# Kernel optimization log

Measured on AMD Instinct MI355X. Metric: run time of the kernel, lower is better.

Reference implementation:

```python
import jax, jax.numpy as jnp
import numpy as np

B, T, IN, OUT = 32, 2048, 1024, 256
DT = 1.0
TAU_MIN, TAU_MAX = 15.0, 25.0


def setup_inputs() -> dict:
    key = jax.random.key(0)
    k1, k2, k3 = jax.random.split(key, 3)
    inputs = jax.random.normal(k1, (B, T, IN), dtype=jnp.float32)
    bound = float(np.sqrt(1.0 / IN))
    weight = jax.random.uniform(k2, (OUT, IN), minval=-bound, maxval=bound, dtype=jnp.float32)
    bias = jnp.zeros((OUT,), dtype=jnp.float32)
    tau = jax.random.uniform(k3, (OUT,), minval=TAU_MIN, maxval=TAU_MAX, dtype=jnp.float32)
    decay = jnp.exp(-DT / tau)  # per-channel leak alpha in (0,1)
    return {"inputs": inputs, "weight": weight, "bias": bias, "decay": decay}


def reference(inputs, weight, bias, decay):
    # Dense projection: [B,T,IN] @ [IN,OUT] -> [B,T,OUT]
    current = jnp.einsum("bti,oi->bto", inputs, weight) + bias
    # Leaky integrator: u_t = alpha * u_{t-1} + (1-alpha) * x_t, u_0 = 0
    one_minus = 1.0 - decay

    def step(u, x):  # u,x: [B,OUT]
        u = decay * u + one_minus * x
        return u, u

    u0 = jnp.zeros((inputs.shape[0], weight.shape[0]), dtype=current.dtype)
    _, us = jax.lax.scan(step, u0, jnp.swapaxes(current, 0, 1))  # [T,B,OUT]
    return jnp.swapaxes(us, 0, 1)  # [B,T,OUT]
```

## Files before the change

kernel.cpp:

```cpp
#include <hip/hip_runtime.h>

#define B_   32
#define T_   2048
#define IN_  1024
#define OUT_ 256
#define M_   (B_ * T_)

#define BM 128
#define BN 256
#define BK 64
#define NSTEPS (IN_ / BK)
#define THREADS 512

#define LC 32
#define NC (T_ / LC)
#define XPAD 264

typedef __attribute__((ext_vector_type(4))) float f32x4;
typedef __attribute__((ext_vector_type(8))) __bf16 bf16x8;

__device__ __forceinline__ unsigned int f2bf_pk(float a, float b) {
    unsigned int ua = __float_as_uint(a);
    unsigned int ub = __float_as_uint(b);
    ua = (ua + 0x7fffu + ((ua >> 16) & 1u)) >> 16;
    ub = (ub + 0x7fffu + ((ub >> 16) & 1u)) >> 16;
    return ua | (ub << 16);
}
__device__ __forceinline__ unsigned short f2bf1(float a) {
    unsigned int ua = __float_as_uint(a);
    return (unsigned short)((ua + 0x7fffu + ((ua >> 16) & 1u)) >> 16);
}
__device__ __forceinline__ float bf2f(unsigned short s) {
    return __uint_as_float((unsigned int)s << 16);
}

__global__ __launch_bounds__(256) void convert_w(const float* __restrict__ W,
                                                 unsigned short* __restrict__ Wb) {
    const int i = blockIdx.x * 256 + threadIdx.x;
    const float4 v = ((const float4*)W)[i];
    uint2 o;
    o.x = f2bf_pk(v.x, v.y);
    o.y = f2bf_pk(v.z, v.w);
    ((uint2*)Wb)[i] = o;
}

__global__ __launch_bounds__(THREADS, 1) void gemm_fused(
    const float* __restrict__ A, const unsigned short* __restrict__ Wb,
    const float* __restrict__ bias, const float* __restrict__ decay,
    unsigned short* __restrict__ Xb, float* __restrict__ chunkend) {
    __shared__ __align__(16) char smem[98304];
#define ABUF(c) ((unsigned short*)(smem + (c) * 16384))
#define BBUF(c) ((unsigned short*)(smem + 32768 + (c) * 32768))

    const int tid  = threadIdx.x;
    const int lane = tid & 63;
    const int wid  = tid >> 6;
    const int wm   = wid >> 2;
    const int wn   = wid & 3;
    const int l15  = lane & 15;
    const int l4   = lane >> 4;
    const int bm0  = blockIdx.x * BM;

    const int gA = tid & 7;
    int rA[2], ldsA[2];
    const float* gsrcA[2];
#pragma unroll
    for (int i = 0; i < 2; ++i) {
        const int q = tid + i * THREADS;
        rA[i] = q >> 3;
        ldsA[i] = rA[i] * BK + ((gA ^ (rA[i] & 7)) << 3);
        gsrcA[i] = A + (size_t)(bm0 + rA[i]) * IN_ + gA * 8;
    }
    int ldsB[4];
    const unsigned short* gsrcB[4];
#pragma unroll
    for (int i = 0; i < 4; ++i) {
        const int q = tid + i * THREADS;
        const int r = q >> 3;
        ldsB[i] = r * BK + ((gA ^ (r & 7)) << 3);
        gsrcB[i] = Wb + (size_t)r * IN_ + gA * 8;
    }

    f32x4 acc[4][4] = {};
    float4 a0[2], a1[2];
    int4 bst[4];

#pragma unroll
    for (int i = 0; i < 2; ++i) {
        a0[i] = *(const float4*)(gsrcA[i]);
        a1[i] = *(const float4*)(gsrcA[i] + 4);
    }
#pragma unroll
    for (int i = 0; i < 4; ++i) bst[i] = *(const int4*)(gsrcB[i]);
#pragma unroll
    for (int i = 0; i < 2; ++i) {
        int4 w;
        w.x = f2bf_pk(a0[i].x, a0[i].y); w.y = f2bf_pk(a0[i].z, a0[i].w);
        w.z = f2bf_pk(a1[i].x, a1[i].y); w.w = f2bf_pk(a1[i].z, a1[i].w);
        *(int4*)&ABUF(0)[ldsA[i]] = w;
    }
#pragma unroll
    for (int i = 0; i < 4; ++i) *(int4*)&BBUF(0)[ldsB[i]] = bst[i];
    __syncthreads();

    int cur = 0;
    for (int step = 0; step < NSTEPS; ++step) {
        const int nxt = step + 1;
        if (nxt < NSTEPS) {
            const int k0 = nxt * BK;
#pragma unroll
            for (int i = 0; i < 2; ++i) {
                a0[i] = *(const float4*)(gsrcA[i] + k0);
                a1[i] = *(const float4*)(gsrcA[i] + k0 + 4);
            }
#pragma unroll
            for (int i = 0; i < 4; ++i) bst[i] = *(const int4*)(gsrcB[i] + k0);
        }
#pragma unroll
        for (int ks = 0; ks < 2; ++ks) {
            bf16x8 af[4], bfv[4];
            const int kg = (ks << 2) + l4;
#pragma unroll
            for (int mi = 0; mi < 4; ++mi) {
                const int row = wm * 64 + mi * 16 + l15;
                af[mi] = *(const bf16x8*)&ABUF(cur)[row * BK + ((kg ^ (row & 7)) << 3)];
            }
#pragma unroll
            for (int ni = 0; ni < 4; ++ni) {
                const int col = wn * 64 + ni * 16 + l15;
                bfv[ni] = *(const bf16x8*)&BBUF(cur)[col * BK + ((kg ^ (col & 7)) << 3)];
            }
#pragma unroll
            for (int mi = 0; mi < 4; ++mi)
#pragma unroll
                for (int ni = 0; ni < 4; ++ni)
                    acc[mi][ni] = __builtin_amdgcn_mfma_f32_16x16x32_bf16(
                        af[mi], bfv[ni], acc[mi][ni], 0, 0, 0);
        }
        if (nxt < NSTEPS) {
#pragma unroll
            for (int i = 0; i < 2; ++i) {
                int4 w;
                w.x = f2bf_pk(a0[i].x, a0[i].y); w.y = f2bf_pk(a0[i].z, a0[i].w);
                w.z = f2bf_pk(a1[i].x, a1[i].y); w.w = f2bf_pk(a1[i].z, a1[i].w);
                *(int4*)&ABUF(cur ^ 1)[ldsA[i]] = w;
            }
#pragma unroll
            for (int i = 0; i < 4; ++i) *(int4*)&BBUF(cur ^ 1)[ldsB[i]] = bst[i];
        }
        __syncthreads();
        cur ^= 1;
    }

    unsigned short* xt = (unsigned short*)smem;
#pragma unroll
    for (int ni = 0; ni < 4; ++ni) {
        const int col = wn * 64 + ni * 16 + l15;
        const float bv = bias[col];
#pragma unroll
        for (int mi = 0; mi < 4; ++mi) {
            const int r0 = wm * 64 + mi * 16 + (l4 << 2);
#pragma unroll
            for (int r = 0; r < 4; ++r)
                xt[(r0 + r) * XPAD + col] = f2bf1(acc[mi][ni][r] + bv);
        }
    }
    __syncthreads();

    const int b  = bm0 >> 11;
    const int c0 = (bm0 >> 5) & 63;

    {
        const int cr = tid >> 5;
        const int cg = (tid & 31) << 3;
#pragma unroll
        for (int it = 0; it < 8; ++it) {
            const int row = it * 16 + cr;
            bf16x8 v = *(const bf16x8*)&xt[row * XPAD + cg];
            *(bf16x8*)&Xb[(size_t)(bm0 + row) * OUT_ + cg] = v;
        }
    }

    for (int task = tid; task < 4 * OUT_; task += THREADS) {
        const int cl  = task >> 8;
        const int col = task & 255;
        const float alpha = decay[col];
        const float om = 1.0f - alpha;
        float u = 0.0f;
        const unsigned short* p = &xt[(cl * LC) * XPAD + col];
#pragma unroll
        for (int t = 0; t < LC; ++t)
            u = fmaf(alpha, u, om * bf2f(p[t * XPAD]));
        chunkend[(size_t)(b * NC + c0 + cl) * OUT_ + col] = u;
    }
#undef ABUF
#undef BBUF
}

__global__ __launch_bounds__(OUT_) void carry_pass(const float* __restrict__ chunkend,
                                                   const float* __restrict__ decay,
                                                   float* __restrict__ carryin) {
    const int b = blockIdx.x;
    const int o = threadIdx.x;
    const float alpha = decay[o];
    float aL = alpha;
#pragma unroll
    for (int i = 1; i < LC; ++i) aL *= alpha;
    float carry = 0.0f;
    for (int c = 0; c < NC; ++c) {
        const size_t idx = (size_t)(b * NC + c) * OUT_ + o;
        carryin[idx] = carry;
        carry = fmaf(aL, carry, chunkend[idx]);
    }
}

__global__ __launch_bounds__(256) void scan_final(const unsigned short* __restrict__ Xb,
                                                  const float* __restrict__ decay,
                                                  const float* __restrict__ carryin,
                                                  float* __restrict__ out) {
    const int unit = blockIdx.x * 4 + (threadIdx.x >> 6);
    const int l    = threadIdx.x & 63;
    const int col  = l << 2;
    const int b    = unit >> 6;
    const int c    = unit & 63;

    const float4 al = *(const float4*)&decay[col];
    const float4 om = {1.0f - al.x, 1.0f - al.y, 1.0f - al.z, 1.0f - al.w};
    float4 u = *(const float4*)&carryin[(size_t)unit * OUT_ + col];

    const size_t base = (size_t)(b * T_ + c * LC) * OUT_ + col;
#pragma unroll 4
    for (int t = 0; t < LC; ++t) {
        const ushort4 xv = *(const ushort4*)&Xb[base + (size_t)t * OUT_];
        u.x = fmaf(al.x, u.x, om.x * bf2f(xv.x));
        u.y = fmaf(al.y, u.y, om.y * bf2f(xv.y));
        u.z = fmaf(al.z, u.z, om.z * bf2f(xv.z));
        u.w = fmaf(al.w, u.w, om.w * bf2f(xv.w));
        *(float4*)&out[base + (size_t)t * OUT_] = u;
    }
}

__global__ __launch_bounds__(256) void gemm_bias(const float* __restrict__ A,
                                                 const float* __restrict__ W,
                                                 const float* __restrict__ bias,
                                                 float* __restrict__ C) {
    __shared__ float As[16][64 + 4];
    __shared__ float Ws[16][64 + 4];
    const int bm = blockIdx.y * 64;
    const int bn = blockIdx.x * 64;
    const int tid = threadIdx.x;
    const int tx = tid & 15, ty = tid >> 4;
    const int lr = tid >> 2, lc = (tid & 3) << 2;
    float acc[4][4] = {};
    const float* Ap = A + (size_t)(bm + lr) * IN_ + lc;
    const float* Wp = W + (size_t)(bn + lr) * IN_ + lc;
    for (int k0 = 0; k0 < IN_; k0 += 16) {
        const float4 a = *(const float4*)(Ap + k0);
        const float4 w = *(const float4*)(Wp + k0);
        __syncthreads();
        As[lc + 0][lr] = a.x; As[lc + 1][lr] = a.y; As[lc + 2][lr] = a.z; As[lc + 3][lr] = a.w;
        Ws[lc + 0][lr] = w.x; Ws[lc + 1][lr] = w.y; Ws[lc + 2][lr] = w.z; Ws[lc + 3][lr] = w.w;
        __syncthreads();
#pragma unroll
        for (int kk = 0; kk < 16; ++kk) {
            const float4 av = *(const float4*)&As[kk][ty << 2];
            const float4 wv = *(const float4*)&Ws[kk][tx << 2];
            const float a0[4] = {av.x, av.y, av.z, av.w};
            const float w0[4] = {wv.x, wv.y, wv.z, wv.w};
#pragma unroll
            for (int i = 0; i < 4; ++i)
#pragma unroll
                for (int j = 0; j < 4; ++j) acc[i][j] = fmaf(a0[i], w0[j], acc[i][j]);
        }
    }
#pragma unroll
    for (int i = 0; i < 4; ++i) {
        const size_t row = (size_t)(bm + (ty << 2) + i);
#pragma unroll
        for (int j = 0; j < 4; ++j)
            C[row * OUT_ + bn + (tx << 2) + j] = acc[i][j] + bias[bn + (tx << 2) + j];
    }
}

__global__ __launch_bounds__(OUT_) void scan_simple(float* __restrict__ C,
                                                    const float* __restrict__ decay) {
    const int b = blockIdx.x;
    const int o = threadIdx.x;
    const float alpha = decay[o];
    const float om = 1.0f - alpha;
    float u = 0.0f;
    float* p = C + (size_t)b * T_ * OUT_ + o;
    for (int t = 0; t < T_; ++t) {
        const float x = p[(size_t)t * OUT_];
        u = fmaf(alpha, u, om * x);
        p[(size_t)t * OUT_] = u;
    }
}

extern "C" void kernel_launch(void* const* d_in, const int* in_sizes, int n_in,
                              void* d_out, int out_size, void* d_ws, size_t ws_size,
                              hipStream_t stream) {
    const float* inputs = (const float*)d_in[0];
    const float* weight = (const float*)d_in[1];
    const float* bias   = (const float*)d_in[2];
    const float* decay  = (const float*)d_in[3];
    float* out = (float*)d_out;

    const size_t wb_bytes = (size_t)OUT_ * IN_ * 2;
    const size_t ce_bytes = (size_t)B_ * NC * OUT_ * 4;
    const size_t ci_bytes = ce_bytes;
    const size_t x_bytes  = (size_t)M_ * OUT_ * 2;
    const size_t need = wb_bytes + ce_bytes + ci_bytes + x_bytes;

    if (ws_size >= need) {
        char* w = (char*)d_ws;
        unsigned short* Wb = (unsigned short*)w;
        float* chunkend    = (float*)(w + wb_bytes);
        float* carryin     = (float*)(w + wb_bytes + ce_bytes);
        unsigned short* Xb = (unsigned short*)(w + wb_bytes + ce_bytes + ci_bytes);

        convert_w<<<(OUT_ * IN_ / 4) / 256, 256, 0, stream>>>(weight, Wb);
        gemm_fused<<<M_ / BM, THREADS, 0, stream>>>(inputs, Wb, bias, decay, Xb, chunkend);
        carry_pass<<<B_, OUT_, 0, stream>>>(chunkend, decay, carryin);
        scan_final<<<(B_ * NC) / 4, 256, 0, stream>>>(Xb, decay, carryin, out);
    } else {
        dim3 g(OUT_ / 64, M_ / 64);
        gemm_bias<<<g, 256, 0, stream>>>(inputs, weight, bias, out);
        scan_simple<<<B_, OUT_, 0, stream>>>(out, decay);
    }
}
```

Baseline: 121.1 us.

## Halve BK, stream weight tiles via global_load_lds, raise occupancy

Reduces the K tile from 64 to 32 and shrinks shared memory to the epilogue staging size, with the GEMM buffers laid out inside it. Raises launch bounds to allow more resident blocks per CU. Loads the bf16 weight tiles straight into LDS with global_load_lds instead of staging them in registers, and adjusts the XOR swizzle for the narrower tile. This frees registers and LDS to improve latency hiding, but doubles the number of K steps and barriers.

```diff
diff --git a/kernel.cpp b/kernel.cpp
--- a/kernel.cpp
+++ b/kernel.cpp
@@ -8,13 +8,17 @@
 
 #define BM 128
 #define BN 256
-#define BK 64
+#define BK 32
 #define NSTEPS (IN_ / BK)
 #define THREADS 512
 
 #define LC 32
 #define NC (T_ / LC)
 #define XPAD 264
+
+#define SMEM_BYTES (BM * XPAD * 2)
+#define ABUF_OFF(c) ((c) * (BM * BK * 2))
+#define BBUF_OFF(c) (2 * (BM * BK * 2) + (c) * (BN * BK * 2))
 
 typedef __attribute__((ext_vector_type(4))) float f32x4;
 typedef __attribute__((ext_vector_type(8))) __bf16 bf16x8;
@@ -32,6 +36,12 @@
 }
 __device__ __forceinline__ float bf2f(unsigned short s) {
     return __uint_as_float((unsigned int)s << 16);
+}
+
+__device__ __forceinline__ void gload_lds16(const void* g, void* l) {
+    __builtin_amdgcn_global_load_lds(
+        (const __attribute__((address_space(1))) void*)g,
+        (__attribute__((address_space(3))) void*)l, 16, 0, 0);
 }
 
 __global__ __launch_bounds__(256) void convert_w(const float* __restrict__ W,
@@ -44,13 +54,11 @@
     ((uint2*)Wb)[i] = o;
 }
 
-__global__ __launch_bounds__(THREADS, 1) void gemm_fused(
+__global__ __launch_bounds__(THREADS, 4) void gemm_fused(
     const float* __restrict__ A, const unsigned short* __restrict__ Wb,
     const float* __restrict__ bias, const float* __restrict__ decay,
     unsigned short* __restrict__ Xb, float* __restrict__ chunkend) {
-    __shared__ __align__(16) char smem[98304];
-#define ABUF(c) ((unsigned short*)(smem + (c) * 16384))
-#define BBUF(c) ((unsigned short*)(smem + 32768 + (c) * 32768))
+    __shared__ __align__(16) char smem[SMEM_BYTES];
 
     const int tid  = threadIdx.x;
     const int lane = tid & 63;
@@ -61,46 +69,36 @@
     const int l4   = lane >> 4;
     const int bm0  = blockIdx.x * BM;
 
-    const int gA = tid & 7;
-    int rA[2], ldsA[2];
-    const float* gsrcA[2];
+    const int rowA = tid >> 2;
+    const int gA   = tid & 3;
+    const float* gsrcA = A + (size_t)(bm0 + rowA) * IN_ + gA * 8;
+    const int ldsA = rowA * BK + ((gA ^ (rowA & 3)) << 3);
+
+    const unsigned short* gsrcB[2];
+    int ldsBbase[2];
 #pragma unroll
     for (int i = 0; i < 2; ++i) {
-        const int q = tid + i * THREADS;
-        rA[i] = q >> 3;
-        ldsA[i] = rA[i] * BK + ((gA ^ (rA[i] & 7)) << 3);
-        gsrcA[i] = A + (size_t)(bm0 + rA[i]) * IN_ + gA * 8;
-    }
-    int ldsB[4];
-    const unsigned short* gsrcB[4];
-#pragma unroll
-    for (int i = 0; i < 4; ++i) {
-        const int q = tid + i * THREADS;
-        const int r = q >> 3;
-        ldsB[i] = r * BK + ((gA ^ (r & 7)) << 3);
-        gsrcB[i] = Wb + (size_t)r * IN_ + gA * 8;
+        const int q = (wid + i * 8) * 64 + lane;
+        const int r = q >> 2;
+        const int g = (q & 3) ^ (r & 3);
+        gsrcB[i] = Wb + (size_t)r * IN_ + g * 8;
+        ldsBbase[i] = (wid + i * 8) * 1024;
     }
 
     f32x4 acc[4][4] = {};
-    float4 a0[2], a1[2];
-    int4 bst[4];
-
-#pragma unroll
-    for (int i = 0; i < 2; ++i) {
-        a0[i] = *(const float4*)(gsrcA[i]);
-        a1[i] = *(const float4*)(gsrcA[i] + 4);
-    }
-#pragma unroll
-    for (int i = 0; i < 4; ++i) bst[i] = *(const int4*)(gsrcB[i]);
-#pragma unroll
-    for (int i = 0; i < 2; ++i) {
+    float4 a0, a1;
+
+#pragma unroll
+    for (int i = 0; i < 2; ++i)
+        gload_lds16(gsrcB[i], smem + BBUF_OFF(0) + ldsBbase[i]);
+    a0 = *(const float4*)(gsrcA);
+    a1 = *(const float4*)(gsrcA + 4);
+    {
         int4 w;
-        w.x = f2bf_pk(a0[i].x, a0[i].y); w.y = f2bf_pk(a0[i].z, a0[i].w);
-        w.z = f2bf_pk(a1[i].x, a1[i].y); w.w = f2bf_pk(a1[i].z, a1[i].w);
-        *(int4*)&ABUF(0)[ldsA[i]] = w;
-    }
-#pragma unroll
-    for (int i = 0; i < 4; ++i) *(int4*)&BBUF(0)[ldsB[i]] = bst[i];
+        w.x = f2bf_pk(a0.x, a0.y); w.y = f2bf_pk(a0.z, a0.w);
+        w.z = f2bf_pk(a1.x, a1.y); w.w = f2bf_pk(a1.z, a1.w);
+        *(int4*)(smem + ABUF_OFF(0) + ldsA * 2) = w;
+    }
     __syncthreads();
 
     int cur = 0;
@@ -109,26 +107,24 @@
         if (nxt < NSTEPS) {
             const int k0 = nxt * BK;
 #pragma unroll
-            for (int i = 0; i < 2; ++i) {
-                a0[i] = *(const float4*)(gsrcA[i] + k0);
-                a1[i] = *(const float4*)(gsrcA[i] + k0 + 4);
-            }
-#pragma unroll
-            for (int i = 0; i < 4; ++i) bst[i] = *(const int4*)(gsrcB[i] + k0);
-        }
-#pragma unroll
-        for (int ks = 0; ks < 2; ++ks) {
+            for (int i = 0; i < 2; ++i)
+                gload_lds16(gsrcB[i] + k0, smem + BBUF_OFF(cur ^ 1) + ldsBbase[i]);
+            a0 = *(const float4*)(gsrcA + k0);
+            a1 = *(const float4*)(gsrcA + k0 + 4);
+        }
+        {
+            const unsigned short* Ab = (const unsigned short*)(smem + ABUF_OFF(cur));
+            const unsigned short* Bb = (const unsigned short*)(smem + BBUF_OFF(cur));
             bf16x8 af[4], bfv[4];
-            const int kg = (ks << 2) + l4;
 #pragma unroll
             for (int mi = 0; mi < 4; ++mi) {
                 const int row = wm * 64 + mi * 16 + l15;
-                af[mi] = *(const bf16x8*)&ABUF(cur)[row * BK + ((kg ^ (row & 7)) << 3)];
+                af[mi] = *(const bf16x8*)&Ab[row * BK + ((l4 ^ (row & 3)) << 3)];
             }
 #pragma unroll
             for (int ni = 0; ni < 4; ++ni) {
                 const int col = wn * 64 + ni * 16 + l15;
-                bfv[ni] = *(const bf16x8*)&BBUF(cur)[col * BK + ((kg ^ (col & 7)) << 3)];
+                bfv[ni] = *(const bf16x8*)&Bb[col * BK + ((l4 ^ (col & 3)) << 3)];
             }
 #pragma unroll
             for (int mi = 0; mi < 4; ++mi)
@@ -138,15 +134,10 @@
                         af[mi], bfv[ni], acc[mi][ni], 0, 0, 0);
         }
         if (nxt < NSTEPS) {
-#pragma unroll
-            for (int i = 0; i < 2; ++i) {
-                int4 w;
-                w.x = f2bf_pk(a0[i].x, a0[i].y); w.y = f2bf_pk(a0[i].z, a0[i].w);
-                w.z = f2bf_pk(a1[i].x, a1[i].y); w.w = f2bf_pk(a1[i].z, a1[i].w);
-                *(int4*)&ABUF(cur ^ 1)[ldsA[i]] = w;
-            }
-#pragma unroll
-            for (int i = 0; i < 4; ++i) *(int4*)&BBUF(cur ^ 1)[ldsB[i]] = bst[i];
+            int4 w;
+            w.x = f2bf_pk(a0.x, a0.y); w.y = f2bf_pk(a0.z, a0.w);
+            w.z = f2bf_pk(a1.x, a1.y); w.w = f2bf_pk(a1.z, a1.w);
+            *(int4*)(smem + ABUF_OFF(cur ^ 1) + ldsA * 2) = w;
         }
         __syncthreads();
         cur ^= 1;
@@ -193,8 +184,6 @@
             u = fmaf(alpha, u, om * bf2f(p[t * XPAD]));
         chunkend[(size_t)(b * NC + c0 + cl) * OUT_ + col] = u;
     }
-#undef ABUF
-#undef BBUF
 }
 
 __global__ __launch_bounds__(OUT_) void carry_pass(const float* __restrict__ chunkend,
```

After: 116.7 us. -3.7%, faster.
